# Performance work log

Measured on AMD Instinct MI355X. Metric: run time of the kernel, lower is better.

The kernel has to match this reference:

```python
import jax, jax.numpy as jnp
import numpy as np

MIN_NORM = 1e-15
BALL_EPS = 1e-5  # keep points strictly inside the unit ball (c = 1)


def _artanh(x):
    return jnp.arctanh(jnp.clip(x, -1.0 + BALL_EPS, 1.0 - BALL_EPS))


def expmap0(u):
    # Poincare ball exp map at the origin, c = 1
    n = jnp.clip(jnp.linalg.norm(u, axis=-1, keepdims=True), MIN_NORM)
    return jnp.tanh(n) * u / n


def mobius_matvec(M, x):
    # Mobius matrix-vector product applied to every row of x: [N, D] -> [N, D]
    x_n = jnp.clip(jnp.linalg.norm(x, axis=-1, keepdims=True), MIN_NORM)
    Mx = x @ M.T
    Mx_n = jnp.clip(jnp.linalg.norm(Mx, axis=-1, keepdims=True), MIN_NORM)
    return jnp.tanh(Mx_n / x_n * _artanh(x_n)) * Mx / Mx_n


def pairwise_sqdist(x):
    # sqdist(x_i, x_j) for all pairs via mobius_add(-x_i, x_j); x: [N, D] -> [N, N]
    u = -x[:, None, :]          # [N, 1, D]
    v = x[None, :, :]           # [1, N, D]
    xy = jnp.sum(u * v, axis=-1, keepdims=True)   # [N, N, 1]
    x2 = jnp.sum(u * u, axis=-1, keepdims=True)
    y2 = jnp.sum(v * v, axis=-1, keepdims=True)
    num = (1.0 + 2.0 * xy + y2) * u + (1.0 - x2) * v   # [N, N, D]
    den = jnp.clip(1.0 + 2.0 * xy + x2 * y2, MIN_NORM)
    ma_n = jnp.linalg.norm(num / den, axis=-1)          # [N, N]
    d = 2.0 * _artanh(ma_n)
    return d * d


def setup_inputs() -> dict:
    key = jax.random.key(0)
    k1, k2, k3 = jax.random.split(key, 3)
    N, D, L = 512, 256, 2
    H_euc = jax.random.normal(k1, (N, D), dtype=jnp.float32)
    att_W = jax.random.normal(k2, (L, D, D), dtype=jnp.float32) / np.sqrt(D)
    A = jax.random.randint(k3, (N, N), 0, 2).astype(bool)
    return {"H_euc": H_euc, "att_W": att_W, "A": A}


def reference(H_euc, att_W, A):
    H = expmap0(H_euc)                      # [N, D] on the Poincare ball
    L = att_W.shape[0]
    for l in range(L):
        Wh = mobius_matvec(att_W[l], H)     # one mobius matvec per node (hoisted out of the i,j loop)
        scores = pairwise_sqdist(Wh)        # [N, N] hyperbolic squared distances
        scores = jnp.where(A, scores, -10000.0)
        att = jax.nn.softmax(scores, axis=1)
        att = jnp.where(A, att, 0.0)
        H = att @ H                         # [N, D]
    return H
```

## Files before the change

kernel.cpp:

```cpp
#include <hip/hip_runtime.h>
#include <math.h>

#define NN 512
#define DD 256

__device__ __forceinline__ void wred_sum2(double& a, double& b){
  #pragma unroll
  for (int o = 32; o > 0; o >>= 1){
    a += __shfl_down(a, o);
    b += __shfl_down(b, o);
  }
}
__device__ void bred_sum2(double& a, double& b){
  __shared__ double sa[4], sb[4]; __shared__ double ra, rb;
  int lane = threadIdx.x & 63, w = threadIdx.x >> 6;
  wred_sum2(a, b);
  __syncthreads();
  if (lane == 0){ sa[w] = a; sb[w] = b; }
  __syncthreads();
  if (threadIdx.x == 0){
    ra = (sa[0] + sa[1]) + (sa[2] + sa[3]);
    rb = (sb[0] + sb[1]) + (sb[2] + sb[3]);
  }
  __syncthreads();
  a = ra; b = rb;
}

__device__ __forceinline__ double artanh_clip(double x){
  const double lim = 1.0 - 1e-5;
  if (x >  lim) x =  lim;
  if (x < -lim) x = -lim;
  return 0.5 * log((1.0 + x) / (1.0 - x));
}

__global__ __launch_bounds__(256) void matvec0_k(
    const float* __restrict__ Hin, const float* __restrict__ W,
    const float* __restrict__ W1, float* __restrict__ W1T,
    float* __restrict__ Hf, float* __restrict__ Wh, float* __restrict__ WhT,
    double* __restrict__ r2){
  __shared__ float h0s[DD], h1s[DD];
  __shared__ float tile[64][65];
  int b = blockIdx.x, t = threadIdx.x;
  int i0 = 2 * b, i1 = i0 + 1;
  float u0 = Hin[i0 * DD + t], u1 = Hin[i1 * DD + t];
  double n0 = (double)u0 * (double)u0, n1 = (double)u1 * (double)u1;
  bred_sum2(n0, n1);
  n0 = sqrt(n0); if (n0 < 1e-15) n0 = 1e-15;
  n1 = sqrt(n1); if (n1 < 1e-15) n1 = 1e-15;
  double t0 = tanh(n0), t1 = tanh(n1);
  float h0 = (float)(t0 / n0 * (double)u0);
  float h1 = (float)(t1 / n1 * (double)u1);
  Hf[i0 * DD + t] = h0; Hf[i1 * DD + t] = h1;
  double xn0 = t0 < 1e-15 ? 1e-15 : t0;
  double xn1 = t1 < 1e-15 ? 1e-15 : t1;
  h0s[t] = h0; h1s[t] = h1;
  __syncthreads();
  const float4* Wt = (const float4*)(W + t * DD);
  const float4* r0 = (const float4*)h0s;
  const float4* r1 = (const float4*)h1s;
  float4 A0 = {0,0,0,0}, A1 = {0,0,0,0};
  #pragma unroll 8
  for (int k = 0; k < DD / 4; k++){
    float4 w = Wt[k], x0 = r0[k], x1 = r1[k];
    A0.x = fmaf(x0.x, w.x, A0.x); A0.y = fmaf(x0.y, w.y, A0.y);
    A0.z = fmaf(x0.z, w.z, A0.z); A0.w = fmaf(x0.w, w.w, A0.w);
    A1.x = fmaf(x1.x, w.x, A1.x); A1.y = fmaf(x1.y, w.y, A1.y);
    A1.z = fmaf(x1.z, w.z, A1.z); A1.w = fmaf(x1.w, w.w, A1.w);
  }
  float mx0 = (A0.x + A0.y) + (A0.z + A0.w);
  float mx1 = (A1.x + A1.y) + (A1.z + A1.w);
  double m0 = (double)mx0 * (double)mx0, m1 = (double)mx1 * (double)mx1;
  bred_sum2(m0, m1);
  double mn0 = sqrt(m0); if (mn0 < 1e-15) mn0 = 1e-15;
  double mn1 = sqrt(m1); if (mn1 < 1e-15) mn1 = 1e-15;
  double th0 = tanh(mn0 / xn0 * artanh_clip(xn0));
  double th1 = tanh(mn1 / xn1 * artanh_clip(xn1));
  float w0 = (float)(mx0 * (th0 / mn0));
  float w1 = (float)(mx1 * (th1 / mn1));
  Wh[i0 * DD + t] = w0;  Wh[i1 * DD + t] = w1;
  WhT[t * NN + i0] = w0; WhT[t * NN + i1] = w1;
  if (t == 0){ r2[i0] = th0 * th0; r2[i1] = th1 * th1; }

  if (b < 16){
    int tr = b >> 2, tc = b & 3;
    int tx = t & 63, ty4 = t >> 6;
    #pragma unroll
    for (int yy = 0; yy < 64; yy += 4)
      tile[yy + ty4][tx] = W1[(tr * 64 + yy + ty4) * DD + tc * 64 + tx];
    __syncthreads();
    #pragma unroll
    for (int yy = 0; yy < 64; yy += 4)
      W1T[(tc * 64 + yy + ty4) * DD + tr * 64 + tx] = tile[tx][yy + ty4];
  }
}

template<bool LAST>
__global__ __launch_bounds__(512) void fused_k(
    const float* __restrict__ Wh, const float* __restrict__ WhT,
    const double* __restrict__ r2, const int* __restrict__ A,
    const float* __restrict__ H, const float* __restrict__ WT2,
    float* __restrict__ Hn, float* __restrict__ Whn,
    float* __restrict__ WhTn, double* __restrict__ r2n){
  int b = blockIdx.x, tid = threadIdx.x;
  int i0 = 2 * b;
  __shared__ float xs[2 * DD];
  __shared__ float a_s[2][NN];
  __shared__ float4 parts[1024];
  __shared__ double ssum[8];
  __shared__ float hn_s[2][DD];
  __shared__ double hnorm2[2];

  xs[tid] = Wh[i0 * DD + tid];
  __syncthreads();

  {
    int ks = tid >> 7, jq = tid & 127;
    const float4* WT4 = (const float4*)WhT;
    const float4* x04 = (const float4*)xs;
    const float4* x14 = (const float4*)(xs + DD);
    float4 p0 = {0,0,0,0}, p1 = {0,0,0,0};
    int kq0 = ks * 16;
    #pragma unroll 4
    for (int kk = 0; kk < 16; kk++){
      float4 xa = x04[kq0 + kk], xb = x14[kq0 + kk];
      const float4* wp = WT4 + (kq0 + kk) * 4 * 128 + jq;
      float4 w0 = wp[0], w1 = wp[128], w2 = wp[256], w3 = wp[384];
      p0.x = fmaf(xa.x, w0.x, p0.x); p0.y = fmaf(xa.x, w0.y, p0.y);
      p0.z = fmaf(xa.x, w0.z, p0.z); p0.w = fmaf(xa.x, w0.w, p0.w);
      p0.x = fmaf(xa.y, w1.x, p0.x); p0.y = fmaf(xa.y, w1.y, p0.y);
      p0.z = fmaf(xa.y, w1.z, p0.z); p0.w = fmaf(xa.y, w1.w, p0.w);
      p0.x = fmaf(xa.z, w2.x, p0.x); p0.y = fmaf(xa.z, w2.y, p0.y);
      p0.z = fmaf(xa.z, w2.z, p0.z); p0.w = fmaf(xa.z, w2.w, p0.w);
      p0.x = fmaf(xa.w, w3.x, p0.x); p0.y = fmaf(xa.w, w3.y, p0.y);
      p0.z = fmaf(xa.w, w3.z, p0.z); p0.w = fmaf(xa.w, w3.w, p0.w);
      p1.x = fmaf(xb.x, w0.x, p1.x); p1.y = fmaf(xb.x, w0.y, p1.y);
      p1.z = fmaf(xb.x, w0.z, p1.z); p1.w = fmaf(xb.x, w0.w, p1.w);
      p1.x = fmaf(xb.y, w1.x, p1.x); p1.y = fmaf(xb.y, w1.y, p1.y);
      p1.z = fmaf(xb.y, w1.z, p1.z); p1.w = fmaf(xb.y, w1.w, p1.w);
      p1.x = fmaf(xb.z, w2.x, p1.x); p1.y = fmaf(xb.z, w2.y, p1.y);
      p1.z = fmaf(xb.z, w2.z, p1.z); p1.w = fmaf(xb.z, w2.w, p1.w);
      p1.x = fmaf(xb.w, w3.x, p1.x); p1.y = fmaf(xb.w, w3.y, p1.y);
      p1.z = fmaf(xb.w, w3.z, p1.z); p1.w = fmaf(xb.w, w3.w, p1.w);
    }
    parts[(ks * 128 + jq) * 2 + 0] = p0;
    parts[(ks * 128 + jq) * 2 + 1] = p1;
  }
  __syncthreads();

  int sgC = tid >> 6, qC = tid & 63;
  const float4* H4 = (const float4*)H;
  float4 hpre[8];
  #pragma unroll
  for (int jj = 0; jj < 8; jj++) hpre[jj] = H4[(sgC * 64 + jj) * 64 + qC];

  int r = tid >> 8, j2 = tid & 255;
  int i = i0 + r;
  double X2 = r2[i];
  const float* pf = (const float*)parts;
  auto dsum = [&](int j) -> double {
    int base = (((j >> 2) * 2 + r) << 2) + (j & 3);
    return ((double)pf[base] + (double)pf[base + 1024])
         + ((double)pf[base + 2048] + (double)pf[base + 3072]);
  };
  double d0 = dsum(j2), d1 = dsum(j2 + 256);

  auto score = [&](double dot, double Y2, int jj) -> double {
    if (i == jj) return 0.0;
    double xy = -dot;
    double a  = 1.0 + 2.0 * xy + Y2;
    double bb = 1.0 - X2;
    double den = 1.0 + 2.0 * xy + X2 * Y2;
    if (den < 1e-15) den = 1e-15;
    double nn = a * a * X2 + 2.0 * a * bb * xy + bb * bb * Y2;
    if (nn < 0.0) nn = 0.0;
    double s = sqrt(nn);
    double smax = den * (1.0 - 1e-5);
    if (s > smax) s = smax;
    double d = log((den + s) / (den - s));
    return d * d;
  };

  double Y0 = r2[j2], Y1 = r2[j2 + 256];
  int m0 = A[i * NN + j2], m1 = A[i * NN + j2 + 256];
  double e0 = 0.0, e1 = 0.0;
  if (m0) e0 = exp(score(d0, Y0, j2) - 150.0);
  if (m1) e1 = exp(score(d1, Y1, j2 + 256) - 150.0);

  double part = e0 + e1;
  #pragma unroll
  for (int o = 32; o > 0; o >>= 1) part += __shfl_down(part, o);
  int w = tid >> 6, lane = tid & 63;
  if (lane == 0) ssum[w] = part;
  __syncthreads();
  int base4 = r * 4;
  double sum = (ssum[base4] + ssum[base4 + 1]) + (ssum[base4 + 2] + ssum[base4 + 3]);
  double inv = 1.0 / sum;
  a_s[r][j2]       = m0 ? (float)(e0 * inv) : 0.f;
  a_s[r][j2 + 256] = m1 ? (float)(e1 * inv) : 0.f;
  __syncthreads();

  {
    float4 c0 = {0,0,0,0}, c1 = {0,0,0,0};
    int jb = sgC * 64;
    #pragma unroll
    for (int jj = 0; jj < 8; jj++){
      int j = jb + jj;
      float a0 = a_s[0][j], a1 = a_s[1][j];
      float4 h = hpre[jj];
      c0.x = fmaf(a0, h.x, c0.x); c0.y = fmaf(a0, h.y, c0.y);
      c0.z = fmaf(a0, h.z, c0.z); c0.w = fmaf(a0, h.w, c0.w);
      c1.x = fmaf(a1, h.x, c1.x); c1.y = fmaf(a1, h.y, c1.y);
      c1.z = fmaf(a1, h.z, c1.z); c1.w = fmaf(a1, h.w, c1.w);
    }
    #pragma unroll 8
    for (int jj = 8; jj < 64; jj++){
      int j = jb + jj;
      float a0 = a_s[0][j], a1 = a_s[1][j];
      float4 h = H4[j * 64 + qC];
      c0.x = fmaf(a0, h.x, c0.x); c0.y = fmaf(a0, h.y, c0.y);
      c0.z = fmaf(a0, h.z, c0.z); c0.w = fmaf(a0, h.w, c0.w);
      c1.x = fmaf(a1, h.x, c1.x); c1.y = fmaf(a1, h.y, c1.y);
      c1.z = fmaf(a1, h.z, c1.z); c1.w = fmaf(a1, h.w, c1.w);
    }
    parts[sgC * 64 + qC]       = c0;
    parts[512 + sgC * 64 + qC] = c1;
  }
  __syncthreads();
  if (tid < 128){
    int rr = tid >> 6, qq = tid & 63;
    float4 p[8];
    #pragma unroll
    for (int s8 = 0; s8 < 8; s8++) p[s8] = parts[rr * 512 + s8 * 64 + qq];
    float4 o;
    o.x = ((p[0].x + p[1].x) + (p[2].x + p[3].x)) + ((p[4].x + p[5].x) + (p[6].x + p[7].x));
    o.y = ((p[0].y + p[1].y) + (p[2].y + p[3].y)) + ((p[4].y + p[5].y) + (p[6].y + p[7].y));
    o.z = ((p[0].z + p[1].z) + (p[2].z + p[3].z)) + ((p[4].z + p[5].z) + (p[6].z + p[7].z));
    o.w = ((p[0].w + p[1].w) + (p[2].w + p[3].w)) + ((p[4].w + p[5].w) + (p[6].w + p[7].w));
    ((float4*)(Hn + (i0 + rr) * DD))[qq] = o;
    if (!LAST){
      ((float4*)hn_s[rr])[qq] = o;
      double s = (double)o.x * o.x + (double)o.y * o.y
               + (double)o.z * o.z + (double)o.w * o.w;
      #pragma unroll
      for (int off = 32; off > 0; off >>= 1) s += __shfl_down(s, off);
      if (qq == 0) hnorm2[rr] = s;
    }
  }
  if (LAST) return;
  __syncthreads();

  {
    int ks2 = tid >> 6, dq = tid & 63;
    const float4* WT4b = (const float4*)WT2;
    const float* h0 = hn_s[0]; const float* h1 = hn_s[1];
    float4 p0 = {0,0,0,0}, p1 = {0,0,0,0};
    int k0 = ks2 * 32;
    #pragma unroll 8
    for (int kk = 0; kk < 32; kk++){
      int k = k0 + kk;
      float4 wv = WT4b[k * 64 + dq];
      float a0v = h0[k], a1v = h1[k];
      p0.x = fmaf(a0v, wv.x, p0.x); p0.y = fmaf(a0v, wv.y, p0.y);
      p0.z = fmaf(a0v, wv.z, p0.z); p0.w = fmaf(a0v, wv.w, p0.w);
      p1.x = fmaf(a1v, wv.x, p1.x); p1.y = fmaf(a1v, wv.y, p1.y);
      p1.z = fmaf(a1v, wv.z, p1.z); p1.w = fmaf(a1v, wv.w, p1.w);
    }
    parts[(ks2 * 64 + dq) * 2 + 0] = p0;
    parts[(ks2 * 64 + dq) * 2 + 1] = p1;
  }
  __syncthreads();
  {
    int rr = tid >> 8, d = tid & 255;
    const float* pf2 = (const float*)parts;
    int base = ((d >> 2) * 2 + rr) * 4 + (d & 3);
    float q0 = pf2[base]        + pf2[base + 512];
    float q1 = pf2[base + 1024] + pf2[base + 1536];
    float q2 = pf2[base + 2048] + pf2[base + 2560];
    float q3 = pf2[base + 3072] + pf2[base + 3584];
    float mx = (q0 + q1) + (q2 + q3);
    double m2 = (double)mx * (double)mx;
    #pragma unroll
    for (int o = 32; o > 0; o >>= 1) m2 += __shfl_down(m2, o);
    int w2 = tid >> 6, lane2 = tid & 63;
    if (lane2 == 0) ssum[w2] = m2;
    __syncthreads();
    int b4 = rr * 4;
    double m2sum = (ssum[b4] + ssum[b4 + 1]) + (ssum[b4 + 2] + ssum[b4 + 3]);
    double mn = sqrt(m2sum); if (mn < 1e-15) mn = 1e-15;
    double xn = sqrt(hnorm2[rr]); if (xn < 1e-15) xn = 1e-15;
    double th = tanh(mn / xn * artanh_clip(xn));
    float wv = (float)((double)mx * (th / mn));
    int irow = i0 + rr;
    Whn[irow * DD + d] = wv;
    WhTn[d * NN + irow] = wv;
    if (d == 0) r2n[irow] = th * th;
  }
}

extern "C" void kernel_launch(void* const* d_in, const int* in_sizes, int n_in,
                              void* d_out, int out_size, void* d_ws, size_t ws_size,
                              hipStream_t stream){
  const float* H_euc = (const float*)d_in[0];
  const float* W     = (const float*)d_in[1];
  const int*   A     = (const int*)d_in[2];
  float* out = (float*)d_out;

  float* Hf   = (float*)d_ws;
  float* Hn   = Hf   + NN * DD;
  float* Wh   = Hn   + NN * DD;
  float* WhT  = Wh   + NN * DD;
  float* Whb  = WhT  + NN * DD;
  float* WhTb = Whb  + NN * DD;
  float* W1T  = WhTb + NN * DD;
  double* r2  = (double*)(W1T + DD * DD);
  double* r2b = r2 + NN;

  matvec0_k<<<NN / 2, DD, 0, stream>>>(H_euc, W, W + DD * DD, W1T, Hf, Wh, WhT, r2);
  fused_k<false><<<NN / 2, 2 * DD, 0, stream>>>(Wh, WhT, r2, A, Hf, W1T, Hn, Whb, WhTb, r2b);
  fused_k<true> <<<NN / 2, 2 * DD, 0, stream>>>(Whb, WhTb, r2b, A, Hn, nullptr, out, nullptr, nullptr, nullptr);
}
```

Baseline: 52.92 us.

## Double fused kernel block size to 1024 threads, one score per thread

Launches the fused attention kernel with 1024 threads per block instead of 512. Each thread now handles one (row, column) score instead of two, and every matvec stage splits its K range across twice as many thread groups. The doubled partial sums are first combined pairwise in shared memory before the final reduction. This adds parallelism per block to hide latency for the 256-block grid, at the cost of more synchronisation, a larger shared-memory footprint, and tighter register limits.

```diff
diff --git a/kernel.cpp b/kernel.cpp
--- a/kernel.cpp
+++ b/kernel.cpp
@@ -3,6 +3,14 @@
 
 #define NN 512
 #define DD 256
+
+#define FMA4(P, S, V) \
+  P.x = fmaf(S, (V).x, P.x); P.y = fmaf(S, (V).y, P.y); \
+  P.z = fmaf(S, (V).z, P.z); P.w = fmaf(S, (V).w, P.w);
+
+__device__ __forceinline__ float4 f4add(float4 a, float4 b){
+  return make_float4(a.x + b.x, a.y + b.y, a.z + b.z, a.w + b.w);
+}
 
 __device__ __forceinline__ void wred_sum2(double& a, double& b){
   #pragma unroll
@@ -75,8 +83,8 @@
   double mn1 = sqrt(m1); if (mn1 < 1e-15) mn1 = 1e-15;
   double th0 = tanh(mn0 / xn0 * artanh_clip(xn0));
   double th1 = tanh(mn1 / xn1 * artanh_clip(xn1));
-  float w0 = (float)(mx0 * (th0 / mn0));
-  float w1 = (float)(mx1 * (th1 / mn1));
+  float w0 = (float)((double)mx0 * (th0 / mn0));
+  float w1 = (float)((double)mx1 * (th1 / mn1));
   Wh[i0 * DD + t] = w0;  Wh[i1 * DD + t] = w1;
   WhT[t * NN + i0] = w0; WhT[t * NN + i1] = w1;
   if (t == 0){ r2[i0] = th0 * th0; r2[i1] = th1 * th1; }
@@ -95,7 +103,7 @@
 }
 
 template<bool LAST>
-__global__ __launch_bounds__(512) void fused_k(
+__global__ __launch_bounds__(1024) void fused_k(
     const float* __restrict__ Wh, const float* __restrict__ WhT,
     const double* __restrict__ r2, const int* __restrict__ A,
     const float* __restrict__ H, const float* __restrict__ WT2,
@@ -105,12 +113,12 @@
   int i0 = 2 * b;
   __shared__ float xs[2 * DD];
   __shared__ float a_s[2][NN];
-  __shared__ float4 parts[1024];
-  __shared__ double ssum[8];
+  __shared__ float4 parts[2048];
+  __shared__ double ssum[16];
   __shared__ float hn_s[2][DD];
   __shared__ double hnorm2[2];
 
-  xs[tid] = Wh[i0 * DD + tid];
+  if (tid < 512) xs[tid] = Wh[i0 * DD + tid];
   __syncthreads();
 
   {
@@ -119,54 +127,45 @@
     const float4* x04 = (const float4*)xs;
     const float4* x14 = (const float4*)(xs + DD);
     float4 p0 = {0,0,0,0}, p1 = {0,0,0,0};
-    int kq0 = ks * 16;
-    #pragma unroll 4
-    for (int kk = 0; kk < 16; kk++){
+    int kq0 = ks * 8;
+    #pragma unroll
+    for (int kk = 0; kk < 8; kk++){
       float4 xa = x04[kq0 + kk], xb = x14[kq0 + kk];
-      const float4* wp = WT4 + (kq0 + kk) * 4 * 128 + jq;
-      float4 w0 = wp[0], w1 = wp[128], w2 = wp[256], w3 = wp[384];
-      p0.x = fmaf(xa.x, w0.x, p0.x); p0.y = fmaf(xa.x, w0.y, p0.y);
-      p0.z = fmaf(xa.x, w0.z, p0.z); p0.w = fmaf(xa.x, w0.w, p0.w);
-      p0.x = fmaf(xa.y, w1.x, p0.x); p0.y = fmaf(xa.y, w1.y, p0.y);
-      p0.z = fmaf(xa.y, w1.z, p0.z); p0.w = fmaf(xa.y, w1.w, p0.w);
-      p0.x = fmaf(xa.z, w2.x, p0.x); p0.y = fmaf(xa.z, w2.y, p0.y);
-      p0.z = fmaf(xa.z, w2.z, p0.z); p0.w = fmaf(xa.z, w2.w, p0.w);
-      p0.x = fmaf(xa.w, w3.x, p0.x); p0.y = fmaf(xa.w, w3.y, p0.y);
-      p0.z = fmaf(xa.w, w3.z, p0.z); p0.w = fmaf(xa.w, w3.w, p0.w);
-      p1.x = fmaf(xb.x, w0.x, p1.x); p1.y = fmaf(xb.x, w0.y, p1.y);
-      p1.z = fmaf(xb.x, w0.z, p1.z); p1.w = fmaf(xb.x, w0.w, p1.w);
-      p1.x = fmaf(xb.y, w1.x, p1.x); p1.y = fmaf(xb.y, w1.y, p1.y);
-      p1.z = fmaf(xb.y, w1.z, p1.z); p1.w = fmaf(xb.y, w1.w, p1.w);
-      p1.x = fmaf(xb.z, w2.x, p1.x); p1.y = fmaf(xb.z, w2.y, p1.y);
-      p1.z = fmaf(xb.z, w2.z, p1.z); p1.w = fmaf(xb.z, w2.w, p1.w);
-      p1.x = fmaf(xb.w, w3.x, p1.x); p1.y = fmaf(xb.w, w3.y, p1.y);
-      p1.z = fmaf(xb.w, w3.z, p1.z); p1.w = fmaf(xb.w, w3.w, p1.w);
-    }
-    parts[(ks * 128 + jq) * 2 + 0] = p0;
-    parts[(ks * 128 + jq) * 2 + 1] = p1;
-  }
-  __syncthreads();
+      const float4* wp = WT4 + (kq0 + kk) * 512 + jq;
+      float4 wa = wp[0], wb = wp[128], wc = wp[256], wd = wp[384];
+      FMA4(p0, xa.x, wa) FMA4(p0, xa.y, wb) FMA4(p0, xa.z, wc) FMA4(p0, xa.w, wd)
+      FMA4(p1, xb.x, wa) FMA4(p1, xb.y, wb) FMA4(p1, xb.z, wc) FMA4(p1, xb.w, wd)
+    }
+    int s4 = ks & 3;
+    int idx = (s4 * 128 + jq) * 2;
+    if (ks >= 4){ parts[idx] = p0; parts[idx + 1] = p1; }
+    __syncthreads();
+    if (ks < 4){
+      parts[idx]     = f4add(p0, parts[idx]);
+      parts[idx + 1] = f4add(p1, parts[idx + 1]);
+    }
+    __syncthreads();
+  }
 
   int sgC = tid >> 6, qC = tid & 63;
   const float4* H4 = (const float4*)H;
   float4 hpre[8];
   #pragma unroll
-  for (int jj = 0; jj < 8; jj++) hpre[jj] = H4[(sgC * 64 + jj) * 64 + qC];
-
-  int r = tid >> 8, j2 = tid & 255;
+  for (int jj = 0; jj < 8; jj++) hpre[jj] = H4[(sgC * 32 + jj) * 64 + qC];
+
+  int r = tid >> 9, j = tid & 511;
   int i = i0 + r;
   double X2 = r2[i];
   const float* pf = (const float*)parts;
-  auto dsum = [&](int j) -> double {
-    int base = (((j >> 2) * 2 + r) << 2) + (j & 3);
-    return ((double)pf[base] + (double)pf[base + 1024])
-         + ((double)pf[base + 2048] + (double)pf[base + 3072]);
-  };
-  double d0 = dsum(j2), d1 = dsum(j2 + 256);
-
-  auto score = [&](double dot, double Y2, int jj) -> double {
-    if (i == jj) return 0.0;
-    double xy = -dot;
+  int basep = (j >> 2) * 8 + r * 4 + (j & 3);
+  double d0 = ((double)pf[basep]        + (double)pf[basep + 1024])
+            + ((double)pf[basep + 2048] + (double)pf[basep + 3072]);
+
+  double e0 = 0.0;
+  int m0 = A[i * NN + j];
+  if (m0 && i != j){
+    double xy = -d0;
+    double Y2 = r2[j];
     double a  = 1.0 + 2.0 * xy + Y2;
     double bb = 1.0 - X2;
     double den = 1.0 + 2.0 * xy + X2 * Y2;
@@ -177,73 +176,63 @@
     double smax = den * (1.0 - 1e-5);
     if (s > smax) s = smax;
     double d = log((den + s) / (den - s));
-    return d * d;
-  };
-
-  double Y0 = r2[j2], Y1 = r2[j2 + 256];
-  int m0 = A[i * NN + j2], m1 = A[i * NN + j2 + 256];
-  double e0 = 0.0, e1 = 0.0;
-  if (m0) e0 = exp(score(d0, Y0, j2) - 150.0);
-  if (m1) e1 = exp(score(d1, Y1, j2 + 256) - 150.0);
-
-  double part = e0 + e1;
+    e0 = exp(d * d - 150.0);
+  } else if (m0){
+    e0 = exp(-150.0);
+  }
+
+  double part = e0;
   #pragma unroll
   for (int o = 32; o > 0; o >>= 1) part += __shfl_down(part, o);
   int w = tid >> 6, lane = tid & 63;
   if (lane == 0) ssum[w] = part;
   __syncthreads();
-  int base4 = r * 4;
-  double sum = (ssum[base4] + ssum[base4 + 1]) + (ssum[base4 + 2] + ssum[base4 + 3]);
-  double inv = 1.0 / sum;
-  a_s[r][j2]       = m0 ? (float)(e0 * inv) : 0.f;
-  a_s[r][j2 + 256] = m1 ? (float)(e1 * inv) : 0.f;
+  int b8 = r * 8;
+  double sum = ((ssum[b8] + ssum[b8+1]) + (ssum[b8+2] + ssum[b8+3]))
+             + ((ssum[b8+4] + ssum[b8+5]) + (ssum[b8+6] + ssum[b8+7]));
+  a_s[r][j] = m0 ? (float)(e0 / sum) : 0.f;
   __syncthreads();
 
   {
     float4 c0 = {0,0,0,0}, c1 = {0,0,0,0};
-    int jb = sgC * 64;
+    int jb = sgC * 32;
     #pragma unroll
     for (int jj = 0; jj < 8; jj++){
-      int j = jb + jj;
-      float a0 = a_s[0][j], a1 = a_s[1][j];
+      int jx = jb + jj;
+      float a0 = a_s[0][jx], a1 = a_s[1][jx];
       float4 h = hpre[jj];
-      c0.x = fmaf(a0, h.x, c0.x); c0.y = fmaf(a0, h.y, c0.y);
-      c0.z = fmaf(a0, h.z, c0.z); c0.w = fmaf(a0, h.w, c0.w);
-      c1.x = fmaf(a1, h.x, c1.x); c1.y = fmaf(a1, h.y, c1.y);
-      c1.z = fmaf(a1, h.z, c1.z); c1.w = fmaf(a1, h.w, c1.w);
+      FMA4(c0, a0, h) FMA4(c1, a1, h)
     }
     #pragma unroll 8
-    for (int jj = 8; jj < 64; jj++){
-      int j = jb + jj;
-      float a0 = a_s[0][j], a1 = a_s[1][j];
-      float4 h = H4[j * 64 + qC];
-      c0.x = fmaf(a0, h.x, c0.x); c0.y = fmaf(a0, h.y, c0.y);
-      c0.z = fmaf(a0, h.z, c0.z); c0.w = fmaf(a0, h.w, c0.w);
-      c1.x = fmaf(a1, h.x, c1.x); c1.y = fmaf(a1, h.y, c1.y);
-      c1.z = fmaf(a1, h.z, c1.z); c1.w = fmaf(a1, h.w, c1.w);
-    }
-    parts[sgC * 64 + qC]       = c0;
-    parts[512 + sgC * 64 + qC] = c1;
-  }
-  __syncthreads();
+    for (int jj = 8; jj < 32; jj++){
+      int jx = jb + jj;
+      float a0 = a_s[0][jx], a1 = a_s[1][jx];
+      float4 h = H4[jx * 64 + qC];
+      FMA4(c0, a0, h) FMA4(c1, a1, h)
+    }
+    int s8 = sgC & 7;
+    int idx = (s8 * 64 + qC) * 2;
+    if (sgC >= 8){ parts[idx] = c0; parts[idx + 1] = c1; }
+    __syncthreads();
+    if (sgC < 8){
+      parts[idx]     = f4add(c0, parts[idx]);
+      parts[idx + 1] = f4add(c1, parts[idx + 1]);
+    }
+    __syncthreads();
+  }
   if (tid < 128){
     int rr = tid >> 6, qq = tid & 63;
-    float4 p[8];
-    #pragma unroll
-    for (int s8 = 0; s8 < 8; s8++) p[s8] = parts[rr * 512 + s8 * 64 + qq];
-    float4 o;
-    o.x = ((p[0].x + p[1].x) + (p[2].x + p[3].x)) + ((p[4].x + p[5].x) + (p[6].x + p[7].x));
-    o.y = ((p[0].y + p[1].y) + (p[2].y + p[3].y)) + ((p[4].y + p[5].y) + (p[6].y + p[7].y));
-    o.z = ((p[0].z + p[1].z) + (p[2].z + p[3].z)) + ((p[4].z + p[5].z) + (p[6].z + p[7].z));
-    o.w = ((p[0].w + p[1].w) + (p[2].w + p[3].w)) + ((p[4].w + p[5].w) + (p[6].w + p[7].w));
+    float4 o = {0,0,0,0};
+    #pragma unroll
+    for (int s = 0; s < 8; s++) o = f4add(o, parts[(s * 64 + qq) * 2 + rr]);
     ((float4*)(Hn + (i0 + rr) * DD))[qq] = o;
     if (!LAST){
       ((float4*)hn_s[rr])[qq] = o;
-      double s = (double)o.x * o.x + (double)o.y * o.y
-               + (double)o.z * o.z + (double)o.w * o.w;
+      double s2 = (double)o.x * o.x + (double)o.y * o.y
+                + (double)o.z * o.z + (double)o.w * o.w;
       #pragma unroll
-      for (int off = 32; off > 0; off >>= 1) s += __shfl_down(s, off);
-      if (qq == 0) hnorm2[rr] = s;
+      for (int off = 32; off > 0; off >>= 1) s2 += __shfl_down(s2, off);
+      if (qq == 0) hnorm2[rr] = s2;
     }
   }
   if (LAST) return;
@@ -254,46 +243,51 @@
     const float4* WT4b = (const float4*)WT2;
     const float* h0 = hn_s[0]; const float* h1 = hn_s[1];
     float4 p0 = {0,0,0,0}, p1 = {0,0,0,0};
-    int k0 = ks2 * 32;
+    int k0 = ks2 * 16;
     #pragma unroll 8
-    for (int kk = 0; kk < 32; kk++){
+    for (int kk = 0; kk < 16; kk++){
       int k = k0 + kk;
       float4 wv = WT4b[k * 64 + dq];
       float a0v = h0[k], a1v = h1[k];
-      p0.x = fmaf(a0v, wv.x, p0.x); p0.y = fmaf(a0v, wv.y, p0.y);
-      p0.z = fmaf(a0v, wv.z, p0.z); p0.w = fmaf(a0v, wv.w, p0.w);
-      p1.x = fmaf(a1v, wv.x, p1.x); p1.y = fmaf(a1v, wv.y, p1.y);
-      p1.z = fmaf(a1v, wv.z, p1.z); p1.w = fmaf(a1v, wv.w, p1.w);
-    }
-    parts[(ks2 * 64 + dq) * 2 + 0] = p0;
-    parts[(ks2 * 64 + dq) * 2 + 1] = p1;
-  }
-  __syncthreads();
+      FMA4(p0, a0v, wv) FMA4(p1, a1v, wv)
+    }
+    int s8 = ks2 & 7;
+    int idx = (s8 * 64 + dq) * 2;
+    if (ks2 >= 8){ parts[idx] = p0; parts[idx + 1] = p1; }
+    __syncthreads();
+    if (ks2 < 8){
+      parts[idx]     = f4add(p0, parts[idx]);
+      parts[idx + 1] = f4add(p1, parts[idx + 1]);
+    }
+    __syncthreads();
+  }
   {
     int rr = tid >> 8, d = tid & 255;
+    float mx = 0.f; double m2 = 0.0;
     const float* pf2 = (const float*)parts;
-    int base = ((d >> 2) * 2 + rr) * 4 + (d & 3);
-    float q0 = pf2[base]        + pf2[base + 512];
-    float q1 = pf2[base + 1024] + pf2[base + 1536];
-    float q2 = pf2[base + 2048] + pf2[base + 2560];
-    float q3 = pf2[base + 3072] + pf2[base + 3584];
-    float mx = (q0 + q1) + (q2 + q3);
-    double m2 = (double)mx * (double)mx;
-    #pragma unroll
-    for (int o = 32; o > 0; o >>= 1) m2 += __shfl_down(m2, o);
-    int w2 = tid >> 6, lane2 = tid & 63;
-    if (lane2 == 0) ssum[w2] = m2;
-    __syncthreads();
-    int b4 = rr * 4;
-    double m2sum = (ssum[b4] + ssum[b4 + 1]) + (ssum[b4 + 2] + ssum[b4 + 3]);
-    double mn = sqrt(m2sum); if (mn < 1e-15) mn = 1e-15;
-    double xn = sqrt(hnorm2[rr]); if (xn < 1e-15) xn = 1e-15;
-    double th = tanh(mn / xn * artanh_clip(xn));
-    float wv = (float)((double)mx * (th / mn));
-    int irow = i0 + rr;
-    Whn[irow * DD + d] = wv;
-    WhTn[d * NN + irow] = wv;
-    if (d == 0) r2n[irow] = th * th;
+    if (tid < 512){
+      int bb = (d >> 2) * 8 + rr * 4 + (d & 3);
+      mx = ((pf2[bb]        + pf2[bb +  512]) + (pf2[bb + 1024] + pf2[bb + 1536]))
+         + ((pf2[bb + 2048] + pf2[bb + 2560]) + (pf2[bb + 3072] + pf2[bb + 3584]));
+      m2 = (double)mx * (double)mx;
+      #pragma unroll
+      for (int o = 32; o > 0; o >>= 1) m2 += __shfl_down(m2, o);
+      int w2 = tid >> 6, lane2 = tid & 63;
+      if (lane2 == 0) ssum[w2] = m2;
+    }
+    __syncthreads();
+    if (tid < 512){
+      int b4 = rr * 4;
+      double m2sum = (ssum[b4] + ssum[b4 + 1]) + (ssum[b4 + 2] + ssum[b4 + 3]);
+      double mn = sqrt(m2sum); if (mn < 1e-15) mn = 1e-15;
+      double xn = sqrt(hnorm2[rr]); if (xn < 1e-15) xn = 1e-15;
+      double th = tanh(mn / xn * artanh_clip(xn));
+      float wv = (float)((double)mx * (th / mn));
+      int irow = i0 + rr;
+      Whn[irow * DD + d] = wv;
+      WhTn[d * NN + irow] = wv;
+      if (d == 0) r2n[irow] = th * th;
+    }
   }
 }
 
@@ -315,7 +309,7 @@
   double* r2  = (double*)(W1T + DD * DD);
   double* r2b = r2 + NN;
 
-  matvec0_k<<<NN / 2, DD, 0, stream>>>(H_euc, W, W + DD * DD, W1T, Hf, Wh, WhT, r2);
-  fused_k<false><<<NN / 2, 2 * DD, 0, stream>>>(Wh, WhT, r2, A, Hf, W1T, Hn, Whb, WhTb, r2b);
-  fused_k<true> <<<NN / 2, 2 * DD, 0, stream>>>(Whb, WhTb, r2b, A, Hn, nullptr, out, nullptr, nullptr, nullptr);
-}
+  matvec0_k<<<NN / 2, 256, 0, stream>>>(H_euc, W, W + DD * DD, W1T, Hf, Wh, WhT, r2);
+  fused_k<false><<<NN / 2, 1024, 0, stream>>>(Wh, WhT, r2, A, Hf, W1T, Hn, Whb, WhTb, r2b);
+  fused_k<true> <<<NN / 2, 1024, 0, stream>>>(Whb, WhTb, r2b, A, Hn, nullptr, out, nullptr, nullptr, nullptr);
+}
```

Result: slower. 54.55 us (+3.1%).
